# Kernel tuning notes

Measured on AMD Instinct MI355X. Metric: run time of the kernel, lower is better.

Reference implementation:

```python
import jax, jax.numpy as jnp
import numpy as np

H, W = 80, 80
LOWPASS = 0.3   # 3DGS low-pass filter added to 2D covariance diagonal
NEAR = 0.2      # near-plane cull depth


def quat_to_rot(q):
    # q: [N,4] (w,x,y,z) -> [N,3,3]
    w, x, y, z = q[..., 0], q[..., 1], q[..., 2], q[..., 3]
    return jnp.stack([
        jnp.stack([1 - 2 * (y * y + z * z), 2 * (x * y - w * z), 2 * (x * z + w * y)], -1),
        jnp.stack([2 * (x * y + w * z), 1 - 2 * (x * x + z * z), 2 * (y * z - w * x)], -1),
        jnp.stack([2 * (x * z - w * y), 2 * (y * z + w * x), 1 - 2 * (x * x + y * y)], -1),
    ], -2)


def setup_inputs() -> dict:
    key = jax.random.key(0)
    k1, k2 = jax.random.split(key)
    vsize = 1.25
    def mids(lo, hi, lim):
        g = np.arange(lo, hi + 1e-6, vsize)
        return ((g[:-1] + g[1:]) / 2.0)[:lim]
    xy = mids(-20.0, 20.0, 200)   # 32 midpoints
    zz = mids(-4.0, 4.0, 16)      # 6 midpoints
    X, Y, Z = np.meshgrid(xy, xy, zz, indexing='ij')
    pc_xyz = jnp.asarray(np.stack([X, Y, Z], -1).reshape(-1, 3), jnp.float32)  # [6144,3]
    N = pc_xyz.shape[0]
    B, NC, C = 1, 6, 32
    vox_features = jax.random.normal(k1, (B, N, C), jnp.float32)
    density = jax.random.normal(k2, (B, N), jnp.float32)
    scales = jnp.full((N, 1), float(np.log(vsize)), jnp.float32)
    rots = jnp.concatenate([jnp.ones((N, 1)), jnp.zeros((N, 3))], -1).astype(jnp.float32)
    # 6 surround cameras at origin, yaw = k*60deg; cam axes: x=right, y=up-ish, z=forward
    yaws = np.arange(NC) * (2 * np.pi / NC)
    f = np.stack([np.cos(yaws), np.sin(yaws), np.zeros(NC)], -1)
    r = np.stack([np.sin(yaws), -np.cos(yaws), np.zeros(NC)], -1)
    u = np.cross(f, r)
    Rw2c = np.stack([r, u, f], 1)  # rows are camera axes -> world2cam rotation [NC,3,3]
    cam_rot = jnp.asarray(Rw2c[None], jnp.float32)          # [B,NC,3,3]
    cam_trans = jnp.zeros((B, NC, 3), jnp.float32)          # [B,NC,3]
    cam_intr = jnp.asarray(np.tile(np.array([45.0, 45.0, W / 2.0, H / 2.0], np.float32), (B, NC, 1)))
    return dict(vox_features=vox_features, density=density, cam_rot=cam_rot,
                cam_trans=cam_trans, cam_intr=cam_intr, pc_xyz=pc_xyz,
                scales=scales, rots=rots)


def _render_one(Rcw, t, intr, pc_xyz, Mcov, opacity, feats):
    # Rcw [3,3], t [3], intr [4]; Mcov [N,3,3] = R*diag(s); opacity [N]; feats [N,C]
    fx, fy, cx, cy = intr[0], intr[1], intr[2], intr[3]
    cam = pc_xyz @ Rcw.T + t                    # [N,3] camera-frame means
    tz = jnp.maximum(cam[:, 2], 1e-6)
    valid = (cam[:, 2] > NEAR).astype(pc_xyz.dtype)
    u = fx * cam[:, 0] / tz + cx
    v = fy * cam[:, 1] / tz + cy
    z0 = jnp.zeros_like(tz)
    J = jnp.stack([jnp.stack([fx / tz, z0, -fx * cam[:, 0] / tz ** 2], -1),
                   jnp.stack([z0, fy / tz, -fy * cam[:, 1] / tz ** 2], -1)], -2)  # [N,2,3]
    A = jnp.einsum('nij,jk->nik', J, Rcw)       # J @ W  [N,2,3]
    Bm = jnp.einsum('nij,njk->nik', A, Mcov)    # [N,2,3]
    cov = jnp.einsum('nij,nkj->nik', Bm, Bm)    # 2D covariance [N,2,2]
    a = cov[:, 0, 0] + LOWPASS
    b = cov[:, 0, 1]
    c = cov[:, 1, 1] + LOWPASS
    det = a * c - b * b
    ia, ib, ic = c / det, -b / det, a / det
    # depth-sort (invalid gaussians pushed to the back)
    order = jnp.argsort(tz + (1.0 - valid) * 1e6)
    u, v, ia, ib, ic = u[order], v[order], ia[order], ib[order], ic[order]
    op_s, feat_s, valid_s = opacity[order], feats[order], valid[order]
    px = jnp.arange(W, dtype=pc_xyz.dtype)
    py = jnp.arange(H, dtype=pc_xyz.dtype)
    dx = px[None, None, :] - u[:, None, None]   # [N,1,W] -> broadcast [N,H,W]
    dy = py[None, :, None] - v[:, None, None]   # [N,H,1]
    power = (-0.5 * (ia[:, None, None] * dx * dx + ic[:, None, None] * dy * dy)
             - ib[:, None, None] * dx * dy)
    g = jnp.exp(jnp.minimum(power, 0.0))
    alpha = jnp.clip(op_s[:, None, None] * g, 0.0, 0.99) * valid_s[:, None, None]
    Tcum = jnp.cumprod(1.0 - alpha, axis=0)
    Texc = jnp.concatenate([jnp.ones((1, H, W), alpha.dtype), Tcum[:-1]], 0)  # exclusive transmittance
    return jnp.einsum('nhw,nc->chw', Texc * alpha, feat_s)


def reference(vox_features, density, cam_rot, cam_trans, cam_intr, pc_xyz, scales, rots):
    Bsz, N, C = vox_features.shape
    Rg = quat_to_rot(rots)                      # [N,3,3]
    s = jnp.exp(scales)                         # [N,1] isotropic scale
    Mcov = Rg * s[:, :, None]                   # R @ diag(s,s,s)
    outs = []
    for b in range(Bsz):
        op = jax.nn.softplus(density[b]).reshape(-1)        # opacity activation
        feats = vox_features[b].reshape(-1, C)
        def rone(args):
            R_, t_, K_ = args
            return _render_one(R_, t_, K_, pc_xyz, Mcov, op, feats)
        out_b = jax.lax.map(rone, (cam_rot[b], cam_trans[b], cam_intr[b]))  # [NC,C,H,W]
        outs.append(out_b)
    return jnp.stack(outs)                      # [B,NC,C,H,W]
```

## Files before the change

### kernel.cpp

```cpp
#include <hip/hip_runtime.h>

#define NEARV    0.2f
#define LOWPASSV 0.3f

constexpr int HH = 80, WW = 80;
constexpr int CFE = 32;
constexpr int NZ = 6;

constexpr int NCELL = 1024;
constexpr int HMAX = NCELL * NZ;

typedef unsigned long long u64;
typedef unsigned int u32;

__global__ __launch_bounds__(256) void prep_kernel(
    const float* __restrict__ pc_xyz, const float* __restrict__ cam_rot,
    const float* __restrict__ cam_trans, const float* __restrict__ cam_intr,
    const float* __restrict__ density, const float* __restrict__ scales,
    int N, int NC,
    int* __restrict__ counts, float4* __restrict__ hdrA,
    float4* __restrict__ hdrB)
{
  __shared__ u32 sk[NCELL];
  __shared__ u32 wred[4];

  const int cam = blockIdx.y;
  const int tid = threadIdx.x;
  const float* R = cam_rot + cam*9;
  const float* t = cam_trans + cam*3;
  const float R20 = R[6], R21 = R[7], R22 = R[8];
  const float t2  = t[2];

  int vcnt = 0;
  #pragma unroll
  for (int e4 = 0; e4 < NCELL/256; ++e4) {
    const int cell = e4*256 + tid;
    const int i0 = cell * NZ;
    u32 key22 = 0x3FFFFFu;
    if (i0 < N) {
      float c2 = R20*pc_xyz[i0*3+0] + R21*pc_xyz[i0*3+1] + R22*pc_xyz[i0*3+2] + t2;
      if (c2 > NEARV) {
        u32 b = __float_as_uint(c2) - 0x3E000000u;
        b = b < 0x03FFFF00u ? b : 0x03FFFF00u;
        key22 = b >> 4;
        ++vcnt;
      }
    }
    sk[cell] = (key22 << 10) | (u32)cell;
  }
  __syncthreads();

  const int e = blockIdx.x * 256 + tid;
  const u32 mykey = sk[e];
  const uint4* k4 = (const uint4*)sk;
  int rank = 0;
  #pragma unroll 8
  for (int i = 0; i < NCELL/4; ++i) {
    const uint4 kv = k4[i];
    rank += (int)(kv.x < mykey) + (int)(kv.y < mykey)
          + (int)(kv.z < mykey) + (int)(kv.w < mykey);
  }

  if (blockIdx.x == 0) {
    #pragma unroll
    for (int off = 32; off > 0; off >>= 1) vcnt += __shfl_down(vcnt, off, 64);
    if ((tid & 63) == 0) wred[tid >> 6] = (u32)vcnt;
    __syncthreads();
    if (tid == 0)
      counts[cam] = (int)(wred[0] + wred[1] + wred[2] + wred[3]) * NZ;
  }

  const float* intr = cam_intr + cam*4;
  const float fx = intr[0], fy = intr[1], cx = intr[2], cy = intr[3];
  const float R0=R[0],R1=R[1],R2=R[2],R3=R[3],R4=R[4],R5=R[5];
  const float t0=t[0],t1=t[1];
  const int b = cam / NC;
  float4* hA = hdrA + (size_t)cam * HMAX;
  float4* hB = hdrB + (size_t)cam * HMAX;

  for (int iz = 0; iz < NZ; ++iz) {
    const int n  = e * NZ + iz;
    const int kq = rank * NZ + iz;
    if (n >= N) break;

    const float p0 = pc_xyz[n*3+0], p1 = pc_xyz[n*3+1], p2 = pc_xyz[n*3+2];
    const float c0 = R0*p0 + R1*p1 + R2*p2 + t0;
    const float c1 = R3*p0 + R4*p1 + R5*p2 + t1;
    const float c2 = R20*p0 + R21*p1 + R22*p2 + t2;
    const float tz = fmaxf(c2, 1e-6f);
    const float itz = 1.0f / tz;
    const float u = fx*c0*itz + cx;
    const float v = fy*c1*itz + cy;
    const float j00 = fx*itz, j02 = -(fx*c0*itz)*itz;
    const float j11 = fy*itz, j12 = -(fy*c1*itz)*itz;
    const float s = expf(scales[n]);
    const float s2 = s*s;
    const float cov00 = s2*(j00*j00 + j02*j02);
    const float cov01 = s2*(j02*j12);
    const float cov11 = s2*(j11*j11 + j12*j12);
    const float a = cov00 + LOWPASSV, bb = cov01, cc = cov11 + LOWPASSV;
    const float det = a*cc - bb*bb;
    const float idet = 1.0f / det;
    const float mid = 0.5f*(a + cc);
    const float dd = sqrtf(fmaxf(mid*mid - det, 0.f));
    float r2 = 32.f * (mid + dd);
    const float dens = density[(size_t)b*N + n];
    const float op = fmaxf(dens, 0.f) + log1pf(expf(-fabsf(dens)));
    const float sx = fminf(fmaxf(u, 0.f), (float)(WW-1)) - u;
    const float sy = fminf(fmaxf(v, 0.f), (float)(HH-1)) - v;
    if (sx*sx + sy*sy > r2) r2 = -1.0f;

    hA[kq] = make_float4(u, v, cc*idet, -bb*idet);
    hB[kq] = make_float4(a*idet, op, r2, __int_as_float(n));
  }
}

__global__ __launch_bounds__(64) void render_kernel(
    const float* __restrict__ vox,
    const float4* __restrict__ hdrA, const float4* __restrict__ hdrB,
    const int* __restrict__ counts,
    float* __restrict__ out, int N, int NC)
{
  __shared__ float4 cA[64], cB[64];
  __shared__ int   cgi[64];
  __shared__ float4 sfeat[64];

  const int cam = blockIdx.y;
  const int tile = blockIdx.x;
  const int tx = tile % (WW/8), ty = tile / (WW/8);
  const int lane = threadIdx.x;
  const int p  = lane & 31;
  const int h  = lane >> 5;
  const int lx = p & 7, ly = p >> 3;
  const int px = tx*8 + lx, py = ty*4 + ly;
  const float fpx = (float)px, fpy = (float)py;
  const float tx0 = (float)(tx*8), tx1 = tx0 + 7.f;
  const float ty0 = (float)(ty*4), ty1 = ty0 + 3.f;
  const int count = counts[cam];
  const int b = cam / NC;
  const float4* hA = hdrA + (size_t)cam * HMAX;
  const float4* hB = hdrB + (size_t)cam * HMAX;
  const float4* voxb = (const float4*)vox + (size_t)b * N * (CFE/4);

  float acc[CFE/2];
  #pragma unroll
  for (int i = 0; i < CFE/2; ++i) acc[i] = 0.f;
  float T = 1.0f;
  bool done = false;

  if (count > 0) {
    const int kcf = min(lane, count - 1);
    float4 na = hA[kcf], nb = hB[kcf];

    for (int k0 = 0; k0 < count && !done; k0 += 64) {
      const float4 a0 = na, b0 = nb;
      if (k0 + 64 < count) {
        const int kn = min(k0 + 64 + lane, count - 1);
        na = hA[kn]; nb = hB[kn];
      }
      const int ki = k0 + lane;
      const float ddx = fminf(fmaxf(a0.x, tx0), tx1) - a0.x;
      const float ddy = fminf(fmaxf(a0.y, ty0), ty1) - a0.y;
      const bool hit = (ki < count) && (ddx*ddx + ddy*ddy <= b0.z);
      const u64 m = __ballot(hit);
      const int P = __popcll(m);
      if (P == 0) continue;
      __syncthreads();
      if (hit) {
        const int pos = (int)__popcll(m & ((1ull << lane) - 1ull));
        cA[pos] = a0;
        cB[pos] = b0;
        cgi[pos] = __float_as_int(b0.w);
      }
      __syncthreads();

      const int sl = lane >> 3, sc = lane & 7;
      float4 pf = voxb[(size_t)cgi[min(sl, P - 1)] * (CFE/4) + sc];

      for (int j = 0; j < P; j += 8) {
        sfeat[lane] = pf;
        if (j + 8 < P) {
          const int si = min(j + 8 + sl, P - 1);
          pf = voxb[(size_t)cgi[si] * (CFE/4) + sc];
        }
        __syncthreads();

        float al[8];
        #pragma unroll
        for (int qq = 0; qq < 8; ++qq) {
          const int idx = j + qq;
          const float4 a1 = cA[idx & 63];
          const float4 a2 = cB[idx & 63];
          const float dx = fpx - a1.x, dy = fpy - a1.y;
          const float power = -0.5f*(a1.z*dx*dx + a2.x*dy*dy) - a1.w*dx*dy;
          float av = fminf(a2.y * __expf(fminf(power, 0.f)), 0.99f);
          av = (power > -16.f) ? av : 0.f;
          al[qq] = (idx < P) ? av : 0.f;
        }
        #pragma unroll
        for (int qq = 0; qq < 8; ++qq) {
          const float w = T * al[qq];
          T -= w;
          if (__any(w > 1e-8f)) {
            const float4* fj = &sfeat[qq * 8 + 4 * h];
            #pragma unroll
            for (int c4 = 0; c4 < 4; ++c4) {
              const float4 fv = fj[c4];
              acc[c4*4+0] += w*fv.x; acc[c4*4+1] += w*fv.y;
              acc[c4*4+2] += w*fv.z; acc[c4*4+3] += w*fv.w;
            }
          }
        }
        if (__all(T < 1e-3f)) { done = true; break; }
        __syncthreads();
      }
    }
  }
  float* ob = out + (((size_t)cam * CFE + 16*h) * HH + py) * WW + px;
  #pragma unroll
  for (int c = 0; c < CFE/2; ++c) ob[(size_t)c * HH * WW] = acc[c];
}

extern "C" void kernel_launch(void* const* d_in, const int* in_sizes, int n_in,
                              void* d_out, int out_size, void* d_ws, size_t ws_size,
                              hipStream_t stream) {
  const float* vox       = (const float*)d_in[0];
  const float* density   = (const float*)d_in[1];
  const float* cam_rot   = (const float*)d_in[2];
  const float* cam_trans = (const float*)d_in[3];
  const float* cam_intr  = (const float*)d_in[4];
  const float* pc_xyz    = (const float*)d_in[5];
  const float* scales    = (const float*)d_in[6];
  float* out = (float*)d_out;

  const int N    = in_sizes[5] / 3;
  const int NCAM = in_sizes[4] / 4;
  const int B    = in_sizes[1] / N;
  const int NC   = NCAM / B;

  unsigned char* ws = (unsigned char*)d_ws;
  int* countsPtr = (int*)ws;
  float4* hdrA   = (float4*)(ws + 32768);
  float4* hdrB   = (float4*)(ws + 32768 + (size_t)NCAM * HMAX * sizeof(float4));

  prep_kernel<<<dim3(NCELL/256, NCAM), 256, 0, stream>>>(
      pc_xyz, cam_rot, cam_trans, cam_intr, density, scales, N, NC,
      countsPtr, hdrA, hdrB);
  render_kernel<<<dim3((WW/8)*(HH/4), NCAM), 64, 0, stream>>>(
      vox, hdrA, hdrB, countsPtr, out, N, NC);
}
```

Measured before the change: 87.74 us.

## Split prep into rank and per-gaussian projection kernels over visible entries

The prep kernel is split in two. A rank kernel only sorts the cells by depth and writes a cell order array. A projection kernel then runs one thread per sorted visible gaussian, rather than one thread looping over 6 z-slices, and skips anything past the visible count. This aims to raise parallelism in the projection stage and avoid work on culled gaussians, at the cost of an extra kernel launch and a global round trip for the cell order.

```diff
diff --git a/kernel.cpp b/kernel.cpp
--- a/kernel.cpp
+++ b/kernel.cpp
@@ -13,13 +13,10 @@
 typedef unsigned long long u64;
 typedef unsigned int u32;
 
-__global__ __launch_bounds__(256) void prep_kernel(
+__global__ __launch_bounds__(256) void rank_kernel(
     const float* __restrict__ pc_xyz, const float* __restrict__ cam_rot,
-    const float* __restrict__ cam_trans, const float* __restrict__ cam_intr,
-    const float* __restrict__ density, const float* __restrict__ scales,
-    int N, int NC,
-    int* __restrict__ counts, float4* __restrict__ hdrA,
-    float4* __restrict__ hdrB)
+    const float* __restrict__ cam_trans, int N,
+    int* __restrict__ counts, int* __restrict__ cellord)
 {
   __shared__ u32 sk[NCELL];
   __shared__ u32 wred[4];
@@ -27,9 +24,8 @@
   const int cam = blockIdx.y;
   const int tid = threadIdx.x;
   const float* R = cam_rot + cam*9;
-  const float* t = cam_trans + cam*3;
   const float R20 = R[6], R21 = R[7], R22 = R[8];
-  const float t2  = t[2];
+  const float t2  = cam_trans[cam*3+2];
 
   int vcnt = 0;
   #pragma unroll
@@ -61,6 +57,8 @@
           + (int)(kv.z < mykey) + (int)(kv.w < mykey);
   }
 
+  cellord[(size_t)cam * NCELL + rank] = e;
+
   if (blockIdx.x == 0) {
     #pragma unroll
     for (int off = 32; off > 0; off >>= 1) vcnt += __shfl_down(vcnt, off, 64);
@@ -69,50 +67,58 @@
     if (tid == 0)
       counts[cam] = (int)(wred[0] + wred[1] + wred[2] + wred[3]) * NZ;
   }
-
+}
+
+__global__ __launch_bounds__(256) void proj_kernel(
+    const float* __restrict__ pc_xyz, const float* __restrict__ cam_rot,
+    const float* __restrict__ cam_trans, const float* __restrict__ cam_intr,
+    const float* __restrict__ density, const float* __restrict__ scales,
+    int N, int NC,
+    const int* __restrict__ counts, const int* __restrict__ cellord,
+    float4* __restrict__ hdrA, float4* __restrict__ hdrB)
+{
+  const int cam = blockIdx.y;
+  const int kq = blockIdx.x * 256 + threadIdx.x;
+  if (kq >= counts[cam]) return;
+
+  const int cellp = kq / NZ;
+  const int n = cellord[(size_t)cam * NCELL + cellp] * NZ + (kq - cellp * NZ);
+
+  const float* R = cam_rot + cam*9;
+  const float* t = cam_trans + cam*3;
   const float* intr = cam_intr + cam*4;
   const float fx = intr[0], fy = intr[1], cx = intr[2], cy = intr[3];
-  const float R0=R[0],R1=R[1],R2=R[2],R3=R[3],R4=R[4],R5=R[5];
-  const float t0=t[0],t1=t[1];
   const int b = cam / NC;
-  float4* hA = hdrA + (size_t)cam * HMAX;
-  float4* hB = hdrB + (size_t)cam * HMAX;
-
-  for (int iz = 0; iz < NZ; ++iz) {
-    const int n  = e * NZ + iz;
-    const int kq = rank * NZ + iz;
-    if (n >= N) break;
-
-    const float p0 = pc_xyz[n*3+0], p1 = pc_xyz[n*3+1], p2 = pc_xyz[n*3+2];
-    const float c0 = R0*p0 + R1*p1 + R2*p2 + t0;
-    const float c1 = R3*p0 + R4*p1 + R5*p2 + t1;
-    const float c2 = R20*p0 + R21*p1 + R22*p2 + t2;
-    const float tz = fmaxf(c2, 1e-6f);
-    const float itz = 1.0f / tz;
-    const float u = fx*c0*itz + cx;
-    const float v = fy*c1*itz + cy;
-    const float j00 = fx*itz, j02 = -(fx*c0*itz)*itz;
-    const float j11 = fy*itz, j12 = -(fy*c1*itz)*itz;
-    const float s = expf(scales[n]);
-    const float s2 = s*s;
-    const float cov00 = s2*(j00*j00 + j02*j02);
-    const float cov01 = s2*(j02*j12);
-    const float cov11 = s2*(j11*j11 + j12*j12);
-    const float a = cov00 + LOWPASSV, bb = cov01, cc = cov11 + LOWPASSV;
-    const float det = a*cc - bb*bb;
-    const float idet = 1.0f / det;
-    const float mid = 0.5f*(a + cc);
-    const float dd = sqrtf(fmaxf(mid*mid - det, 0.f));
-    float r2 = 32.f * (mid + dd);
-    const float dens = density[(size_t)b*N + n];
-    const float op = fmaxf(dens, 0.f) + log1pf(expf(-fabsf(dens)));
-    const float sx = fminf(fmaxf(u, 0.f), (float)(WW-1)) - u;
-    const float sy = fminf(fmaxf(v, 0.f), (float)(HH-1)) - v;
-    if (sx*sx + sy*sy > r2) r2 = -1.0f;
-
-    hA[kq] = make_float4(u, v, cc*idet, -bb*idet);
-    hB[kq] = make_float4(a*idet, op, r2, __int_as_float(n));
-  }
+
+  const float p0 = pc_xyz[n*3+0], p1 = pc_xyz[n*3+1], p2 = pc_xyz[n*3+2];
+  const float c0 = R[0]*p0 + R[1]*p1 + R[2]*p2 + t[0];
+  const float c1 = R[3]*p0 + R[4]*p1 + R[5]*p2 + t[1];
+  const float c2 = R[6]*p0 + R[7]*p1 + R[8]*p2 + t[2];
+  const float tz = fmaxf(c2, 1e-6f);
+  const float itz = 1.0f / tz;
+  const float u = fx*c0*itz + cx;
+  const float v = fy*c1*itz + cy;
+  const float j00 = fx*itz, j02 = -(fx*c0*itz)*itz;
+  const float j11 = fy*itz, j12 = -(fy*c1*itz)*itz;
+  const float s = expf(scales[n]);
+  const float s2 = s*s;
+  const float cov00 = s2*(j00*j00 + j02*j02);
+  const float cov01 = s2*(j02*j12);
+  const float cov11 = s2*(j11*j11 + j12*j12);
+  const float a = cov00 + LOWPASSV, bb = cov01, cc = cov11 + LOWPASSV;
+  const float det = a*cc - bb*bb;
+  const float idet = 1.0f / det;
+  const float mid = 0.5f*(a + cc);
+  const float dd = sqrtf(fmaxf(mid*mid - det, 0.f));
+  float r2 = 32.f * (mid + dd);
+  const float dens = density[(size_t)b*N + n];
+  const float op = fmaxf(dens, 0.f) + log1pf(expf(-fabsf(dens)));
+  const float sx = fminf(fmaxf(u, 0.f), (float)(WW-1)) - u;
+  const float sy = fminf(fmaxf(v, 0.f), (float)(HH-1)) - v;
+  if (sx*sx + sy*sy > r2) r2 = -1.0f;
+
+  hdrA[(size_t)cam * HMAX + kq] = make_float4(u, v, cc*idet, -bb*idet);
+  hdrB[(size_t)cam * HMAX + kq] = make_float4(a*idet, op, r2, __int_as_float(n));
 }
 
 __global__ __launch_bounds__(64) void render_kernel(
@@ -240,12 +246,15 @@
 
   unsigned char* ws = (unsigned char*)d_ws;
   int* countsPtr = (int*)ws;
+  int* cellord   = (int*)(ws + 256);
   float4* hdrA   = (float4*)(ws + 32768);
   float4* hdrB   = (float4*)(ws + 32768 + (size_t)NCAM * HMAX * sizeof(float4));
 
-  prep_kernel<<<dim3(NCELL/256, NCAM), 256, 0, stream>>>(
+  rank_kernel<<<dim3(NCELL/256, NCAM), 256, 0, stream>>>(
+      pc_xyz, cam_rot, cam_trans, N, countsPtr, cellord);
+  proj_kernel<<<dim3((HMAX + 255) / 256, NCAM), 256, 0, stream>>>(
       pc_xyz, cam_rot, cam_trans, cam_intr, density, scales, N, NC,
-      countsPtr, hdrA, hdrB);
+      countsPtr, cellord, hdrA, hdrB);
   render_kernel<<<dim3((WW/8)*(HH/4), NCAM), 64, 0, stream>>>(
       vox, hdrA, hdrB, countsPtr, out, N, NC);
 }
```

Result: faster. 85.12 us (-3.0%).
